# Optimization experiments

Hardware: AMD Instinct MI355X
Metric: run time of the kernel (lower is better)

## Reference

```python
import jax, jax.numpy as jnp
import numpy as np

BS = 2; D = 256; NH = 8; NL = 4; NP = 4; WS = 7; DFF = 1024
SHAPES = [(92, 92), (46, 46), (23, 23), (12, 12)]
LEN = sum(h * w for h, w in SHAPES)  # 11253
DH = D // NH


def _layer_norm(x, g, b):
    mu = jnp.mean(x, -1, keepdims=True)
    var = jnp.var(x, -1, keepdims=True)
    return (x - mu) * jax.lax.rsqrt(var + 1e-5) * g + b


def _bilinear(v_l, loc, H_, W_):
    # v_l: (N, nh, H_*W_, d); loc: (N, Lq, nh, P, 2) normalized in [0,1] (x, y)
    N, Lq, nh, P, _ = loc.shape
    x = loc[..., 0] * W_ - 0.5  # grid_sample align_corners=False convention
    y = loc[..., 1] * H_ - 0.5
    x0f = jnp.floor(x); y0f = jnp.floor(y)
    tx = (x - x0f).transpose(0, 2, 1, 3)  # (N, nh, Lq, P)
    ty = (y - y0f).transpose(0, 2, 1, 3)
    x0 = x0f.astype(jnp.int32).transpose(0, 2, 1, 3)
    y0 = y0f.astype(jnp.int32).transpose(0, 2, 1, 3)

    def g(yi, xi):
        valid = ((xi >= 0) & (xi < W_) & (yi >= 0) & (yi < H_)).astype(v_l.dtype)
        idx = (jnp.clip(yi, 0, H_ - 1) * W_ + jnp.clip(xi, 0, W_ - 1)).reshape(N, nh, Lq * P)
        out = jnp.take_along_axis(v_l, idx[..., None], axis=2).reshape(N, nh, Lq, P, -1)
        return out * valid[..., None]

    return (g(y0, x0) * ((1 - tx) * (1 - ty))[..., None]
            + g(y0, x0 + 1) * (tx * (1 - ty))[..., None]
            + g(y0 + 1, x0) * ((1 - tx) * ty)[..., None]
            + g(y0 + 1, x0 + 1) * (tx * ty)[..., None])


def setup_inputs() -> dict:
    key = jax.random.key(0)
    ks = jax.random.split(key, 20)
    s = 0.02
    inp = {}
    inp['src'] = jax.random.normal(ks[0], (BS, LEN, D), jnp.float32)
    inp['pos'] = jax.random.normal(ks[1], (BS, LEN, D), jnp.float32)
    inp['reference_points'] = jax.random.uniform(ks[2], (BS, LEN, NL, 2), jnp.float32)
    c = WS // 2
    ys, xs = jnp.meshgrid(jnp.arange(WS) - c, jnp.arange(WS) - c, indexing='ij')
    inp['window_grid'] = jnp.stack([xs, ys], -1).reshape(WS * WS, 2).astype(jnp.float32)
    for l, (h, w) in enumerate(SHAPES):
        inp[f'mask{l}'] = jax.random.normal(ks[3 + l], (BS, 1, h, w), jnp.float32)
    inp['spatial_shapes'] = jnp.array(SHAPES, jnp.int32)
    starts = np.cumsum([0] + [h * w for h, w in SHAPES])[:NL]
    inp['level_start_index'] = jnp.array(starts, jnp.int32)
    # parse_mask: Conv2d(1, n_heads, 1) per level -> per-head scale + bias
    inp['pm_w'] = jax.random.normal(ks[7], (NL, NH), jnp.float32) * s
    inp['pm_b'] = jax.random.normal(ks[8], (NL, NH), jnp.float32) * s
    inp['Wv'] = jax.random.normal(ks[9], (D, D), jnp.float32) * s
    inp['bv'] = jnp.zeros((D,), jnp.float32)
    inp['Wo'] = jax.random.normal(ks[10], (D, D), jnp.float32) * s
    inp['bo'] = jnp.zeros((D,), jnp.float32)
    inp['ln1_g'] = jnp.ones((D,), jnp.float32)
    inp['ln1_b'] = jnp.zeros((D,), jnp.float32)
    inp['W1'] = jax.random.normal(ks[11], (D, DFF), jnp.float32) * s
    inp['b1'] = jnp.zeros((DFF,), jnp.float32)
    inp['W2'] = jax.random.normal(ks[12], (DFF, D), jnp.float32) * s
    inp['b2'] = jnp.zeros((D,), jnp.float32)
    inp['ln2_g'] = jnp.ones((D,), jnp.float32)
    inp['ln2_b'] = jnp.zeros((D,), jnp.float32)
    return inp


def reference(src, pos, reference_points, window_grid, mask0, mask1, mask2, mask3,
              spatial_shapes, level_start_index, pm_w, pm_b, Wv, bv, Wo, bo,
              ln1_g, ln1_b, W1, b1, W2, b2, ln2_g, ln2_b):
    masks = [mask0, mask1, mask2, mask3]
    p = WS // 2
    offs, samp = [], []
    for l, (H_, W_) in enumerate(SHAPES):
        # 1x1 conv from 1 -> NH channels
        m = masks[l] * pm_w[l][None, :, None, None] + pm_b[l][None, :, None, None]  # (BS,NH,H,W)
        mp = jnp.pad(m, ((0, 0), (0, 0), (p, p), (p, p)))
        # unfold: (BS, NH, WS*WS, H*W), kernel positions row-major
        patches = jnp.stack([mp[:, :, i:i + H_, j:j + W_] for i in range(WS) for j in range(WS)], axis=2)
        patches = patches.reshape(BS, NH, WS * WS, H_ * W_).transpose(0, 1, 3, 2)  # (BS,NH,HW,WS^2)
        vals, idx = jax.lax.top_k(patches, NP)  # (BS,NH,HW,NP)
        off = window_grid[idx]  # (BS,NH,HW,NP,2)
        offs.append(off.transpose(0, 2, 1, 3, 4))   # (BS,HW,NH,NP,2)
        samp.append(vals.transpose(0, 2, 1, 3))     # (BS,HW,NH,NP)
    offsets = jnp.concatenate(offs, axis=1)       # (BS,LEN,NH,NP,2)
    pred_sampled = jnp.concatenate(samp, axis=1)  # (BS,LEN,NH,NP)

    # MSDeformAttn (encoder mode: external offsets + mask-derived attention logits)
    value = (src @ Wv + bv).reshape(BS, LEN, NH, DH)
    attn = jax.nn.softmax(
        jnp.broadcast_to(pred_sampled[:, :, :, None, :], (BS, LEN, NH, NL, NP)).reshape(BS, LEN, NH, NL * NP),
        axis=-1).reshape(BS, LEN, NH, NL, NP)
    norm = jnp.array([[w, h] for h, w in SHAPES], jnp.float32)  # (NL, 2) as (W, H)
    loc = reference_points[:, :, None, :, None, :] + offsets[:, :, :, None, :, :] / norm[None, None, None, :, None, :]

    out = jnp.zeros((BS, LEN, NH, DH), src.dtype)
    s0 = 0
    for l, (H_, W_) in enumerate(SHAPES):
        v_l = value[:, s0:s0 + H_ * W_].transpose(0, 2, 1, 3)  # (BS,NH,HW,DH)
        sampled = _bilinear(v_l, loc[:, :, :, l], H_, W_)       # (BS,NH,LEN,NP,DH)
        out = out + jnp.einsum('nhqpd,nqhp->nqhd', sampled, attn[:, :, :, l])
        s0 += H_ * W_
    attn_out = out.reshape(BS, LEN, D) @ Wo + bo

    x = _layer_norm(src + attn_out, ln1_g, ln1_b)
    x2 = jax.nn.relu(x @ W1 + b1) @ W2 + b2
    return _layer_norm(x + x2, ln2_g, ln2_b)
```

## Files before the change

kernel.cpp:

```cpp
#include <hip/hip_runtime.h>
#include <cstddef>
#include <cstdint>

#define LEN_T 11253
#define TOK   22506
#define NHEADS 8
#define DMODEL 256

typedef __attribute__((ext_vector_type(8))) short short8;
typedef __attribute__((ext_vector_type(4))) float f32x4;

__device__ __forceinline__ unsigned short f2bf(float f) {
  union { float f; unsigned u; } v; v.f = f;
  unsigned r = v.u + 0x7fffu + ((v.u >> 16) & 1u);
  return (unsigned short)(r >> 16);
}
__device__ __forceinline__ float bfhi2f(unsigned u) {
  union { unsigned u; float f; } v; v.u = u & 0xffff0000u; return v.f;
}
__device__ __forceinline__ float bflo2f(unsigned u) {
  union { unsigned u; float f; } v; v.u = u << 16; return v.f;
}

__device__ __forceinline__ void gld_lds16(const void* g, void* l) {
  __builtin_amdgcn_global_load_lds(
      (const __attribute__((address_space(1))) void*)g,
      (__attribute__((address_space(3))) void*)l, 16, 0, 0);
}

__global__ __launch_bounds__(256) void pre_kernel(
    const float* __restrict__ m0, const float* __restrict__ m1,
    const float* __restrict__ m2, const float* __restrict__ m3,
    const float* __restrict__ pm_w, const float* __restrict__ pm_b,
    const float* __restrict__ Wv, const float* __restrict__ Wo,
    const float* __restrict__ W1, const float* __restrict__ W2,
    unsigned short* __restrict__ Wv_t, unsigned short* __restrict__ Wo_t,
    unsigned short* __restrict__ W1_t, unsigned short* __restrict__ W2_t,
    unsigned* __restrict__ offp, float* __restrict__ attw)
{
  int blk = blockIdx.x;
  if (blk >= 704) {
    int cb = blk - 704;
    const float* W; unsigned short* Bt; int lk, ln, i;
    if (cb < 256)       { W = Wv; Bt = Wv_t; lk = 8;  ln = 8;  i = cb * 256 + threadIdx.x; }
    else if (cb < 512)  { W = Wo; Bt = Wo_t; lk = 8;  ln = 8;  i = (cb - 256) * 256 + threadIdx.x; }
    else if (cb < 1536) { W = W1; Bt = W1_t; lk = 8;  ln = 10; i = (cb - 512) * 256 + threadIdx.x; }
    else                { W = W2; Bt = W2_t; lk = 10; ln = 8;  i = (cb - 1536) * 256 + threadIdx.x; }
    int n = i >> lk;
    int k = i & ((1 << lk) - 1);
    Bt[i] = f2bf(W[((size_t)k << ln) + n]);
    return;
  }
  int t = blk * 256 + threadIdx.x;
  if (t >= TOK * NHEADS) return;
  int h  = t & 7;
  int bq = t >> 3;
  int b  = bq / LEN_T;
  int q  = bq - b * LEN_T;
  int l, H_, W_;
  const float* mk;
  if (q < 8464)       { l = 0; H_ = 92; W_ = 92; mk = m0; }
  else if (q < 10580) { l = 1; H_ = 46; W_ = 46; mk = m1; }
  else if (q < 11109) { l = 2; H_ = 23; W_ = 23; mk = m2; }
  else                { l = 3; H_ = 12; W_ = 12; mk = m3; }
  int st = (l == 0) ? 0 : (l == 1) ? 8464 : (l == 2) ? 10580 : 11109;
  int pos = q - st;
  int rr = pos / W_;
  int cc = pos - rr * W_;
  float w  = pm_w[l * NHEADS + h];
  float bb = pm_b[l * NHEADS + h];
  const float* mp = mk + (size_t)b * H_ * W_;

  float bestv[4] = {-1e30f, -1e30f, -1e30f, -1e30f};
  int   bestk[4] = {0, 0, 0, 0};
  for (int k = 0; k < 49; ++k) {
    int i = k / 7, j = k - (k / 7) * 7;
    int yy = rr + i - 3, xx = cc + j - 3;
    float v = 0.f;
    if (yy >= 0 && yy < H_ && xx >= 0 && xx < W_) v = mp[yy * W_ + xx] * w + bb;
    if (v > bestv[3]) {
      int p4 = 3;
      while (p4 > 0 && v > bestv[p4 - 1]) {
        bestv[p4] = bestv[p4 - 1]; bestk[p4] = bestk[p4 - 1]; --p4;
      }
      bestv[p4] = v; bestk[p4] = k;
    }
  }
  float mx = bestv[0];
  float ee[4];
  float s = 0.f;
  #pragma unroll
  for (int p = 0; p < 4; ++p) { ee[p] = __expf(bestv[p] - mx); s += ee[p]; }
  float inv = 1.f / (4.f * s);
  unsigned pk = 0;
  float* wp = attw + (size_t)t * 4;
  #pragma unroll
  for (int p = 0; p < 4; ++p) {
    int k = bestk[p];
    int i = k / 7, j = k - i * 7;
    pk |= (unsigned)(j | (i << 4)) << (8 * p);
    wp[p] = ee[p] * inv;
  }
  offp[t] = pk;
}

__global__ __launch_bounds__(256) void sample_kernel(
    const unsigned short* __restrict__ Vb, const float* __restrict__ refpts,
    const unsigned* __restrict__ offp, const float* __restrict__ attw,
    unsigned short* __restrict__ outp)
{
  __shared__ int4  sidx[4][128];
  __shared__ float4 swgt[4][128];
  const int wv   = threadIdx.x >> 6;
  const int lane = threadIdx.x & 63;
  const int bx = blockIdx.x & 7, by = blockIdx.x >> 3;
  const int nb = bx * 703 + min(bx, 3) + by;
  const int blk = nb * 4 + wv;
  const bool ok = blk < TOK;

  if (ok) {
    const int b = (blk >= LEN_T) ? 1 : 0;
    const float* rp = refpts + (size_t)blk * 8;
    #pragma unroll
    for (int e = 0; e < 2; ++e) {
      int t = lane * 2 + e;
      int h = t & 7, lp = t >> 3;
      int l = lp >> 2, p = lp & 3;
      unsigned pb = (offp[(size_t)blk * 8 + h] >> (8 * p)) & 0xffu;
      float ox = (float)(int)(pb & 15u) - 3.f;
      float oy = (float)(int)(pb >> 4)  - 3.f;
      float aw = attw[((size_t)blk * 8 + h) * 4 + p];
      int H_ = (l == 0) ? 92 : (l == 1) ? 46 : (l == 2) ? 23 : 12;
      int st = (l == 0) ? 0  : (l == 1) ? 8464 : (l == 2) ? 10580 : 11109;
      float xx = rp[2 * l]     * (float)H_ - 0.5f + ox;
      float yy = rp[2 * l + 1] * (float)H_ - 0.5f + oy;
      float x0f = floorf(xx), y0f = floorf(yy);
      float tx = xx - x0f, ty = yy - y0f;
      int x0 = (int)x0f, y0 = (int)y0f;
      int base = b * LEN_T + st;
      float wc[4] = {(1.f - tx) * (1.f - ty), tx * (1.f - ty),
                     (1.f - tx) * ty,         tx * ty};
      int4 idx; float4 wg;
      int xs[4] = {x0, x0 + 1, x0, x0 + 1};
      int ys[4] = {y0, y0, y0 + 1, y0 + 1};
      int   id[4]; float wgt[4];
      #pragma unroll
      for (int c = 0; c < 4; ++c) {
        int xi = xs[c], yi = ys[c];
        bool v_ = (xi >= 0) & (xi < H_) & (yi >= 0) & (yi < H_);
        id[c]  = base + min(max(yi, 0), H_ - 1) * H_ + min(max(xi, 0), H_ - 1);
        wgt[c] = v_ ? aw * wc[c] : 0.f;
      }
      idx.x = id[0]; idx.y = id[1]; idx.z = id[2]; idx.w = id[3];
      wg.x = wgt[0]; wg.y = wgt[1]; wg.z = wgt[2]; wg.w = wgt[3];
      sidx[wv][t] = idx;
      swgt[wv][t] = wg;
    }
  }
  __syncthreads();

  if (ok) {
    const int h = lane >> 3, dg = lane & 7;
    const unsigned short* vb = Vb + h * 32 + dg * 4;
    f32x4 acc = {0.f, 0.f, 0.f, 0.f};
    #pragma unroll 4
    for (int lp = 0; lp < 16; ++lp) {
      int4  idx = sidx[wv][lp * 8 + h];
      float4 wg = swgt[wv][lp * 8 + h];
      uint2 u0 = *(const uint2*)(vb + (size_t)idx.x * DMODEL);
      uint2 u1 = *(const uint2*)(vb + (size_t)idx.y * DMODEL);
      uint2 u2 = *(const uint2*)(vb + (size_t)idx.z * DMODEL);
      uint2 u3 = *(const uint2*)(vb + (size_t)idx.w * DMODEL);
      acc.x += wg.x * bflo2f(u0.x) + wg.y * bflo2f(u1.x) + wg.z * bflo2f(u2.x) + wg.w * bflo2f(u3.x);
      acc.y += wg.x * bfhi2f(u0.x) + wg.y * bfhi2f(u1.x) + wg.z * bfhi2f(u2.x) + wg.w * bfhi2f(u3.x);
      acc.z += wg.x * bflo2f(u0.y) + wg.y * bflo2f(u1.y) + wg.z * bflo2f(u2.y) + wg.w * bflo2f(u3.y);
      acc.w += wg.x * bfhi2f(u0.y) + wg.y * bfhi2f(u1.y) + wg.z * bfhi2f(u2.y) + wg.w * bfhi2f(u3.y);
    }
    uint2 o;
    o.x = (unsigned)f2bf(acc.x) | ((unsigned)f2bf(acc.y) << 16);
    o.y = (unsigned)f2bf(acc.z) | ((unsigned)f2bf(acc.w) << 16);
    *(uint2*)(outp + (size_t)blk * DMODEL + h * 32 + dg * 4) = o;
  }
}

template<int EPI, bool AF32>
__global__ __launch_bounds__(256, 2) void gemm_k256(
    const void* __restrict__ Aptr, const short* __restrict__ Bt,
    const float* __restrict__ bias, const float* __restrict__ res,
    const float* __restrict__ lng, const float* __restrict__ lnb,
    float* __restrict__ C, unsigned short* __restrict__ Cb,
    int M, int N)
{
  __shared__ short As[2][64 * 32] __attribute__((aligned(16)));
  __shared__ float2 lnred[64][4];
  const int tid  = threadIdx.x;
  const int w    = tid >> 6;
  const int lane = tid & 63;
  const int row0 = blockIdx.x * 64;
  const int wn   = blockIdx.y * 256 + w * 64;
  const int colq = lane & 15, quad = lane >> 4;
  const int kq8  = quad * 8;

  short8 bq[8][4];
  #pragma unroll
  for (int kc = 0; kc < 8; ++kc)
    #pragma unroll
    for (int nt = 0; nt < 4; ++nt)
      bq[kc][nt] = *(const short8*)(Bt + (size_t)(wn + nt * 16 + colq) * 256
                                       + kc * 32 + kq8);

  f32x4 acc[4][4];
  #pragma unroll
  for (int i = 0; i < 4; ++i)
    #pragma unroll
    for (int j = 0; j < 4; ++j) acc[i][j] = (f32x4){0.f, 0.f, 0.f, 0.f};

  const int rA  = min(row0 + (tid >> 2), M - 1);
  const int kq4 = (tid & 3) * 8;
  const float* Af = (const float*)Aptr;
  const short* Ab = (const short*)Aptr;

  auto stageA = [&](int kb, int nbuf) {
    if constexpr (AF32) {
      const float* ap = Af + (size_t)rA * 256 + kb * 32 + kq4;
      float4 f0 = *(const float4*)ap;
      float4 f1 = *(const float4*)(ap + 4);
      uint4 u;
      u.x = (unsigned)f2bf(f0.x) | ((unsigned)f2bf(f0.y) << 16);
      u.y = (unsigned)f2bf(f0.z) | ((unsigned)f2bf(f0.w) << 16);
      u.z = (unsigned)f2bf(f1.x) | ((unsigned)f2bf(f1.y) << 16);
      u.w = (unsigned)f2bf(f1.z) | ((unsigned)f2bf(f1.w) << 16);
      *(uint4*)(As[nbuf] + (size_t)tid * 8) = u;
    } else {
      gld_lds16(Ab + (size_t)rA * 256 + kb * 32 + kq4, As[nbuf] + (size_t)tid * 8);
    }
  };

  stageA(0, 0);
  __syncthreads();
  int buf = 0;
  #pragma unroll
  for (int kb = 0; kb < 8; ++kb) {
    if (kb < 7) stageA(kb + 1, buf ^ 1);
    short8 af[4];
    #pragma unroll
    for (int mt = 0; mt < 4; ++mt)
      af[mt] = *(const short8*)(As[buf] + (size_t)(mt * 16 + colq) * 32 + kq8);
    #pragma unroll
    for (int mt = 0; mt < 4; ++mt)
      #pragma unroll
      for (int nt = 0; nt < 4; ++nt)
        acc[mt][nt] = __builtin_amdgcn_mfma_f32_16x16x32_bf16(
            af[mt], bq[kb][nt], acc[mt][nt], 0, 0, 0);
    __syncthreads();
    buf ^= 1;
  }

  float bia[4];
  #pragma unroll
  for (int nt = 0; nt < 4; ++nt) bia[nt] = bias[wn + nt * 16 + colq];

  if constexpr (EPI == 1) {
    #pragma unroll
    for (int mt = 0; mt < 4; ++mt) {
      #pragma unroll
      for (int r = 0; r < 4; ++r) {
        int lrow = mt * 16 + quad * 4 + r;
        int rowc = min(row0 + lrow, M - 1);
        float s = 0.f, sq = 0.f;
        #pragma unroll
        for (int nt = 0; nt < 4; ++nt) {
          float f = acc[mt][nt][r] + bia[nt]
                  + res[(size_t)rowc * 256 + wn + nt * 16 + colq];
          acc[mt][nt][r] = f;
          s += f; sq += f * f;
        }
        #pragma unroll
        for (int off = 1; off < 16; off <<= 1) {
          s  += __shfl_xor(s,  off, 64);
          sq += __shfl_xor(sq, off, 64);
        }
        if (colq == 0) lnred[lrow][w] = (float2){s, sq};
      }
    }
    __syncthreads();
    #pragma unroll
    for (int mt = 0; mt < 4; ++mt) {
      #pragma unroll
      for (int r = 0; r < 4; ++r) {
        int lrow = mt * 16 + quad * 4 + r;
        int row  = row0 + lrow;
        if (row >= M) continue;
        float2 p0 = lnred[lrow][0], p1 = lnred[lrow][1];
        float2 p2 = lnred[lrow][2], p3 = lnred[lrow][3];
        float mu  = (p0.x + p1.x + p2.x + p3.x) * (1.f / 256.f);
        float var = (p0.y + p1.y + p2.y + p3.y) * (1.f / 256.f) - mu * mu;
        float rs  = rsqrtf(var + 1e-5f);
        #pragma unroll
        for (int nt = 0; nt < 4; ++nt) {
          int col = wn + nt * 16 + colq;
          float o = (acc[mt][nt][r] - mu) * rs * lng[col] + lnb[col];
          C[(size_t)row * 256 + col]  = o;
          Cb[(size_t)row * 256 + col] = f2bf(o);
        }
      }
    }
  } else {
    #pragma unroll
    for (int mt = 0; mt < 4; ++mt) {
      #pragma unroll
      for (int r = 0; r < 4; ++r) {
        int row = row0 + mt * 16 + quad * 4 + r;
        if (row < M) {
          #pragma unroll
          for (int nt = 0; nt < 4; ++nt) {
            float f = acc[mt][nt][r] + bia[nt];
            if constexpr (EPI == 2) f = fmaxf(f, 0.f);
            Cb[(size_t)row * N + wn + nt * 16 + colq] = f2bf(f);
          }
        }
      }
    }
  }
}

__global__ __launch_bounds__(256) void gemm_n256_ln(
    const short* __restrict__ A, const short* __restrict__ Bt,
    const float* __restrict__ bias, const float* __restrict__ res,
    const float* __restrict__ lng, const float* __restrict__ lnb,
    float* __restrict__ C, int M, int K)
{
  __shared__ short As[64 * 32]  __attribute__((aligned(16)));
  __shared__ short Bs[256 * 32] __attribute__((aligned(16)));
  __shared__ float2 lnred[64][2];
  const int tid  = threadIdx.x;
  const int w    = tid >> 6;
  const int lane = tid & 63;
  const int row0 = blockIdx.x * 64;

  f32x4 acc[2][8];
  #pragma unroll
  for (int i = 0; i < 2; ++i)
    #pragma unroll
    for (int j = 0; j < 8; ++j) acc[i][j] = (f32x4){0.f, 0.f, 0.f, 0.f};

  const int rA = min(row0 + (tid >> 2), M - 1);
  const short* ap = A + (size_t)rA * K + (tid & 3) * 8;
  short* lA = As + tid * 8;
  const short* bp[4]; short* lB[4];
  #pragma unroll
  for (int c = 0; c < 4; ++c) {
    int rB = c * 64 + (tid >> 2);
    bp[c] = Bt + (size_t)rB * K + (tid & 3) * 8;
    lB[c] = Bs + c * 2048 + tid * 8;
  }
  const int wm = (w & 1) * 32, wn = (w >> 1) * 128;
  const short* Abase = As + (size_t)(wm + (lane & 15)) * 32 + (lane >> 4) * 8;
  const short* Bbase = Bs + (size_t)(wn + (lane & 15)) * 32 + (lane >> 4) * 8;

  for (int kb = 0; kb < K; kb += 32) {
    gld_lds16(ap + kb, lA);
    #pragma unroll
    for (int c = 0; c < 4; ++c) gld_lds16(bp[c] + kb, lB[c]);
    __syncthreads();
    short8 af[2], bfr[8];
    #pragma unroll
    for (int mt = 0; mt < 2; ++mt) af[mt]  = *(const short8*)(Abase + mt * 16 * 32);
    #pragma unroll
    for (int nt = 0; nt < 8; ++nt) bfr[nt] = *(const short8*)(Bbase + nt * 16 * 32);
    #pragma unroll
    for (int mt = 0; mt < 2; ++mt)
      #pragma unroll
      for (int nt = 0; nt < 8; ++nt)
        acc[mt][nt] = __builtin_amdgcn_mfma_f32_16x16x32_bf16(
            af[mt], bfr[nt], acc[mt][nt], 0, 0, 0);
    __syncthreads();
  }

  const int colq = lane & 15, quad = lane >> 4;
  float bia[8];
  #pragma unroll
  for (int nt = 0; nt < 8; ++nt) bia[nt] = bias[wn + nt * 16 + colq];

  #pragma unroll
  for (int mt = 0; mt < 2; ++mt) {
    #pragma unroll
    for (int r = 0; r < 4; ++r) {
      int lrow = wm + mt * 16 + quad * 4 + r;
      int rowc = min(row0 + lrow, M - 1);
      float s = 0.f, sq = 0.f;
      #pragma unroll
      for (int nt = 0; nt < 8; ++nt) {
        float f = acc[mt][nt][r] + bia[nt]
                + res[(size_t)rowc * 256 + wn + nt * 16 + colq];
        acc[mt][nt][r] = f;
        s += f; sq += f * f;
      }
      #pragma unroll
      for (int off = 1; off < 16; off <<= 1) {
        s  += __shfl_xor(s,  off, 64);
        sq += __shfl_xor(sq, off, 64);
      }
      if (colq == 0) lnred[lrow][w >> 1] = (float2){s, sq};
    }
  }
  __syncthreads();
  #pragma unroll
  for (int mt = 0; mt < 2; ++mt) {
    #pragma unroll
    for (int r = 0; r < 4; ++r) {
      int lrow = wm + mt * 16 + quad * 4 + r;
      int row  = row0 + lrow;
      if (row >= M) continue;
      float2 p0 = lnred[lrow][0], p1 = lnred[lrow][1];
      float mu  = (p0.x + p1.x) * (1.f / 256.f);
      float var = (p0.y + p1.y) * (1.f / 256.f) - mu * mu;
      float rs  = rsqrtf(var + 1e-5f);
      #pragma unroll
      for (int nt = 0; nt < 8; ++nt) {
        int col = wn + nt * 16 + colq;
        C[(size_t)row * 256 + col] =
            (acc[mt][nt][r] - mu) * rs * lng[col] + lnb[col];
      }
    }
  }
}

extern "C" void kernel_launch(void* const* d_in, const int* in_sizes, int n_in,
                              void* d_out, int out_size, void* d_ws, size_t ws_size,
                              hipStream_t stream)
{
  const float* src    = (const float*)d_in[0];
  const float* refpts = (const float*)d_in[2];
  const float* m0   = (const float*)d_in[4];
  const float* m1   = (const float*)d_in[5];
  const float* m2   = (const float*)d_in[6];
  const float* m3   = (const float*)d_in[7];
  const float* pm_w = (const float*)d_in[10];
  const float* pm_b = (const float*)d_in[11];
  const float* Wv   = (const float*)d_in[12];
  const float* bv   = (const float*)d_in[13];
  const float* Wo   = (const float*)d_in[14];
  const float* bo   = (const float*)d_in[15];
  const float* W1   = (const float*)d_in[18];
  const float* b1   = (const float*)d_in[19];
  const float* W2   = (const float*)d_in[20];
  const float* b2   = (const float*)d_in[21];
  const float* ln1g = (const float*)d_in[16];
  const float* ln1b = (const float*)d_in[17];
  const float* ln2g = (const float*)d_in[22];
  const float* ln2b = (const float*)d_in[23];
  float* out = (float*)d_out;
  char*  w   = (char*)d_ws;

  const bool big = ws_size >= 97096256ull;
  const size_t H1SZ = big ? 46092288ull : 23046144ull;

  unsigned short* Vb      = (unsigned short*)(w);
  unsigned short* attnpre = (unsigned short*)(w + 11523072);
  float*          xf32    = (float*)(w + 23046144);
  unsigned short* h1      = (unsigned short*)(w + 46092288);
  char*           tail    = w + 46092288 + H1SZ;
  float*          attw    = (float*)(tail);
  unsigned*       offp    = (unsigned*)(tail + 2880768);
  unsigned short* Wv_t    = (unsigned short*)(tail + 3600960);
  unsigned short* Wo_t    = (unsigned short*)(tail + 3732032);
  unsigned short* W1_t    = (unsigned short*)(tail + 3863104);
  unsigned short* W2_t    = (unsigned short*)(tail + 4387392);
  unsigned short* x_bf    = attnpre;

  pre_kernel<<<dim3(3264), 256, 0, stream>>>(
      m0, m1, m2, m3, pm_w, pm_b, Wv, Wo, W1, W2,
      Wv_t, Wo_t, W1_t, W2_t, offp, attw);

  gemm_k256<0, true><<<dim3(352, 1), 256, 0, stream>>>(
      src, (const short*)Wv_t, bv, nullptr, nullptr, nullptr,
      nullptr, Vb, TOK, 256);

  sample_kernel<<<dim3(5627), 256, 0, stream>>>(
      Vb, refpts, offp, attw, attnpre);

  gemm_k256<1, false><<<dim3(352, 1), 256, 0, stream>>>(
      attnpre, (const short*)Wo_t, bo, src, ln1g, ln1b,
      xf32, x_bf, TOK, 256);

  if (big) {
    gemm_k256<2, false><<<dim3(352, 4), 256, 0, stream>>>(
        x_bf, (const short*)W1_t, b1, nullptr, nullptr, nullptr,
        nullptr, h1, TOK, 1024);
    gemm_n256_ln<<<dim3(352), 256, 0, stream>>>(
        (const short*)h1, (const short*)W2_t, b2, xf32, ln2g, ln2b,
        out, TOK, 1024);
  } else {
    for (int ch = 0; ch < 2; ++ch) {
      const unsigned short* xc = x_bf + (size_t)ch * LEN_T * 256;
      const float*          xr = xf32 + (size_t)ch * LEN_T * 256;
      float*                oc = out  + (size_t)ch * LEN_T * 256;
      gemm_k256<2, false><<<dim3(176, 4), 256, 0, stream>>>(
          xc, (const short*)W1_t, b1, nullptr, nullptr, nullptr,
          nullptr, h1, LEN_T, 1024);
      gemm_n256_ln<<<dim3(176), 256, 0, stream>>>(
          (const short*)h1, (const short*)W2_t, b2, xr, ln2g, ln2b,
          oc, LEN_T, 1024);
    }
  }
}
```

Baseline: 338.6 us.

## Restructure mask top-k, sampling, and FFN2 GEMM with register-resident B

The pre-kernel now handles one token per thread. For interior windows it computes the top-4 and bottom-4 of the 7x7 mask neighbourhood once and reuses them for all 8 heads, picking by the sign of the head weight (the bias cancels inside the softmax). Weight transposes write four elements per thread. The sampling kernel processes two tokens per wave with 16-byte value loads, 16-bit LDS indices, and occupancy hint 3. The separate FFN2 LDS-tiled GEMM is replaced by the register-resident-B GEMM generalised over K in chunks, which reloads B per 256-wide chunk. The trade-off is more register pressure and reloading B from global memory in FFN2.

```diff
diff --git a/kernel.cpp b/kernel.cpp
--- a/kernel.cpp
+++ b/kernel.cpp
@@ -21,11 +21,21 @@
 __device__ __forceinline__ float bflo2f(unsigned u) {
   union { unsigned u; float f; } v; v.u = u << 16; return v.f;
 }
-
 __device__ __forceinline__ void gld_lds16(const void* g, void* l) {
   __builtin_amdgcn_global_load_lds(
       (const __attribute__((address_space(1))) void*)g,
       (__attribute__((address_space(3))) void*)l, 16, 0, 0);
+}
+
+__device__ __forceinline__ void ins4(float v, int ji,
+    float& t0, float& t1, float& t2, float& t3,
+    int& i0, int& i1, int& i2, int& i3)
+{
+  bool a0 = v > t0, a1 = v > t1, a2 = v > t2, a3 = v > t3;
+  t3 = a3 ? (a2 ? t2 : v) : t3;  i3 = a3 ? (a2 ? i2 : ji) : i3;
+  t2 = a2 ? (a1 ? t1 : v) : t2;  i2 = a2 ? (a1 ? i1 : ji) : i2;
+  t1 = a1 ? (a0 ? t0 : v) : t1;  i1 = a1 ? (a0 ? i0 : ji) : i1;
+  t0 = a0 ? v : t0;              i0 = a0 ? ji : i0;
 }
 
 __global__ __launch_bounds__(256) void pre_kernel(
@@ -39,24 +49,28 @@
     unsigned* __restrict__ offp, float* __restrict__ attw)
 {
   int blk = blockIdx.x;
-  if (blk >= 704) {
-    int cb = blk - 704;
-    const float* W; unsigned short* Bt; int lk, ln, i;
-    if (cb < 256)       { W = Wv; Bt = Wv_t; lk = 8;  ln = 8;  i = cb * 256 + threadIdx.x; }
-    else if (cb < 512)  { W = Wo; Bt = Wo_t; lk = 8;  ln = 8;  i = (cb - 256) * 256 + threadIdx.x; }
-    else if (cb < 1536) { W = W1; Bt = W1_t; lk = 8;  ln = 10; i = (cb - 512) * 256 + threadIdx.x; }
-    else                { W = W2; Bt = W2_t; lk = 10; ln = 8;  i = (cb - 1536) * 256 + threadIdx.x; }
-    int n = i >> lk;
-    int k = i & ((1 << lk) - 1);
-    Bt[i] = f2bf(W[((size_t)k << ln) + n]);
+  if (blk >= 88) {
+    int cb = blk - 88;
+    const float* W; unsigned short* Bt; int lk, ln, base;
+    if (cb < 64)       { W = Wv; Bt = Wv_t; lk = 8;  ln = 8;  base = cb; }
+    else if (cb < 128) { W = Wo; Bt = Wo_t; lk = 8;  ln = 8;  base = cb - 64; }
+    else if (cb < 384) { W = W1; Bt = W1_t; lk = 8;  ln = 10; base = cb - 128; }
+    else               { W = W2; Bt = W2_t; lk = 10; ln = 8;  base = cb - 384; }
+    int i4 = (base * 256 + threadIdx.x) * 4;
+    int n  = i4 >> lk;
+    int k  = i4 & ((1 << lk) - 1);
+    ushort4 o;
+    o.x = f2bf(W[((size_t)(k + 0) << ln) + n]);
+    o.y = f2bf(W[((size_t)(k + 1) << ln) + n]);
+    o.z = f2bf(W[((size_t)(k + 2) << ln) + n]);
+    o.w = f2bf(W[((size_t)(k + 3) << ln) + n]);
+    *(ushort4*)(Bt + i4) = o;
     return;
   }
-  int t = blk * 256 + threadIdx.x;
-  if (t >= TOK * NHEADS) return;
-  int h  = t & 7;
-  int bq = t >> 3;
-  int b  = bq / LEN_T;
-  int q  = bq - b * LEN_T;
+  int tok = blk * 256 + threadIdx.x;
+  if (tok >= TOK) return;
+  int b = tok >= LEN_T;
+  int q = tok - b * LEN_T;
   int l, H_, W_;
   const float* mk;
   if (q < 8464)       { l = 0; H_ = 92; W_ = 92; mk = m0; }
@@ -67,130 +81,168 @@
   int pos = q - st;
   int rr = pos / W_;
   int cc = pos - rr * W_;
-  float w  = pm_w[l * NHEADS + h];
-  float bb = pm_b[l * NHEADS + h];
   const float* mp = mk + (size_t)b * H_ * W_;
-
-  float bestv[4] = {-1e30f, -1e30f, -1e30f, -1e30f};
-  int   bestk[4] = {0, 0, 0, 0};
-  for (int k = 0; k < 49; ++k) {
-    int i = k / 7, j = k - (k / 7) * 7;
-    int yy = rr + i - 3, xx = cc + j - 3;
-    float v = 0.f;
-    if (yy >= 0 && yy < H_ && xx >= 0 && xx < W_) v = mp[yy * W_ + xx] * w + bb;
-    if (v > bestv[3]) {
-      int p4 = 3;
-      while (p4 > 0 && v > bestv[p4 - 1]) {
-        bestv[p4] = bestv[p4 - 1]; bestk[p4] = bestk[p4 - 1]; --p4;
-      }
-      bestv[p4] = v; bestk[p4] = k;
-    }
-  }
-  float mx = bestv[0];
-  float ee[4];
-  float s = 0.f;
-  #pragma unroll
-  for (int p = 0; p < 4; ++p) { ee[p] = __expf(bestv[p] - mx); s += ee[p]; }
-  float inv = 1.f / (4.f * s);
-  unsigned pk = 0;
-  float* wp = attw + (size_t)t * 4;
-  #pragma unroll
-  for (int p = 0; p < 4; ++p) {
-    int k = bestk[p];
-    int i = k / 7, j = k - i * 7;
-    pk |= (unsigned)(j | (i << 4)) << (8 * p);
-    wp[p] = ee[p] * inv;
-  }
-  offp[t] = pk;
-}
-
-__global__ __launch_bounds__(256) void sample_kernel(
+  bool interior = (rr >= 3) && (rr + 3 < H_) && (cc >= 3) && (cc + 3 < W_);
+
+  if (interior) {
+    float t0=-1e30f,t1=-1e30f,t2=-1e30f,t3=-1e30f; int ti0=0,ti1=0,ti2=0,ti3=0;
+    float n0=-1e30f,n1=-1e30f,n2=-1e30f,n3=-1e30f; int bi0=0,bi1=0,bi2=0,bi3=0;
+    for (int i = 0; i < 7; ++i) {
+      const float* rowp = mp + (size_t)(rr + i - 3) * W_ + cc - 3;
+      #pragma unroll
+      for (int j = 0; j < 7; ++j) {
+        float v = rowp[j];
+        int ji = j | (i << 4);
+        ins4(v,  ji, t0, t1, t2, t3, ti0, ti1, ti2, ti3);
+        ins4(-v, ji, n0, n1, n2, n3, bi0, bi1, bi2, bi3);
+      }
+    }
+    unsigned pkt = (unsigned)ti0 | ((unsigned)ti1 << 8) | ((unsigned)ti2 << 16) | ((unsigned)ti3 << 24);
+    unsigned pkb = (unsigned)bi0 | ((unsigned)bi1 << 8) | ((unsigned)bi2 << 16) | ((unsigned)bi3 << 24);
+    #pragma unroll
+    for (int h = 0; h < 8; ++h) {
+      float w = pm_w[l * NHEADS + h];
+      bool neg = w < 0.f;
+      float v0 = neg ? -n0 : t0, v1 = neg ? -n1 : t1;
+      float v2 = neg ? -n2 : t2, v3 = neg ? -n3 : t3;
+      float e1 = __expf(w * (v1 - v0));
+      float e2 = __expf(w * (v2 - v0));
+      float e3 = __expf(w * (v3 - v0));
+      float inv = 1.f / (4.f * (1.f + e1 + e2 + e3));
+      float4 wout; wout.x = inv; wout.y = e1 * inv; wout.z = e2 * inv; wout.w = e3 * inv;
+      *(float4*)(attw + ((size_t)tok * 8 + h) * 4) = wout;
+      offp[(size_t)tok * 8 + h] = neg ? pkb : pkt;
+    }
+  } else {
+    #pragma unroll 1
+    for (int h = 0; h < 8; ++h) {
+      float w  = pm_w[l * NHEADS + h];
+      float bb = pm_b[l * NHEADS + h];
+      float t0=-1e30f,t1=-1e30f,t2=-1e30f,t3=-1e30f; int i0=0,i1=0,i2=0,i3=0;
+      for (int i = 0; i < 7; ++i) {
+        int yy = rr + i - 3;
+        #pragma unroll
+        for (int j = 0; j < 7; ++j) {
+          int xx = cc + j - 3;
+          float v = 0.f;
+          if (yy >= 0 && yy < H_ && xx >= 0 && xx < W_)
+            v = mp[(size_t)yy * W_ + xx] * w + bb;
+          ins4(v, j | (i << 4), t0, t1, t2, t3, i0, i1, i2, i3);
+        }
+      }
+      float e1 = __expf(t1 - t0);
+      float e2 = __expf(t2 - t0);
+      float e3 = __expf(t3 - t0);
+      float inv = 1.f / (4.f * (1.f + e1 + e2 + e3));
+      float4 wout; wout.x = inv; wout.y = e1 * inv; wout.z = e2 * inv; wout.w = e3 * inv;
+      *(float4*)(attw + ((size_t)tok * 8 + h) * 4) = wout;
+      offp[(size_t)tok * 8 + h] = (unsigned)i0 | ((unsigned)i1 << 8)
+                                | ((unsigned)i2 << 16) | ((unsigned)i3 << 24);
+    }
+  }
+}
+
+__global__ __launch_bounds__(256, 3) void sample_kernel(
     const unsigned short* __restrict__ Vb, const float* __restrict__ refpts,
     const unsigned* __restrict__ offp, const float* __restrict__ attw,
     unsigned short* __restrict__ outp)
 {
-  __shared__ int4  sidx[4][128];
-  __shared__ float4 swgt[4][128];
+  __shared__ ushort4 sidx[4][2][128];
+  __shared__ float4  swgt[4][2][128];
   const int wv   = threadIdx.x >> 6;
   const int lane = threadIdx.x & 63;
   const int bx = blockIdx.x & 7, by = blockIdx.x >> 3;
-  const int nb = bx * 703 + min(bx, 3) + by;
-  const int blk = nb * 4 + wv;
-  const bool ok = blk < TOK;
-
-  if (ok) {
-    const int b = (blk >= LEN_T) ? 1 : 0;
-    const float* rp = refpts + (size_t)blk * 8;
-    #pragma unroll
-    for (int e = 0; e < 2; ++e) {
-      int t = lane * 2 + e;
-      int h = t & 7, lp = t >> 3;
-      int l = lp >> 2, p = lp & 3;
-      unsigned pb = (offp[(size_t)blk * 8 + h] >> (8 * p)) & 0xffu;
+  const int nb = bx * 351 + min(bx, 6) + by;
+  const int base = nb * 8;
+
+  #pragma unroll
+  for (int e = 0; e < 4; ++e) {
+    int g  = lane * 4 + e;
+    int tk = g >> 7, t = g & 127;
+    int token = base + wv * 2 + tk;
+    ushort4 idx; idx.x = 0; idx.y = 0; idx.z = 0; idx.w = 0;
+    float4  wg;  wg.x = 0.f; wg.y = 0.f; wg.z = 0.f; wg.w = 0.f;
+    if (token < TOK) {
+      int h = t & 7, lp = t >> 3, lev = lp >> 2, p = lp & 3;
+      int b = token >= LEN_T;
+      unsigned pb = (offp[(size_t)token * 8 + h] >> (8 * p)) & 0xffu;
+      float aw = attw[((size_t)token * 8 + h) * 4 + p];
       float ox = (float)(int)(pb & 15u) - 3.f;
       float oy = (float)(int)(pb >> 4)  - 3.f;
-      float aw = attw[((size_t)blk * 8 + h) * 4 + p];
-      int H_ = (l == 0) ? 92 : (l == 1) ? 46 : (l == 2) ? 23 : 12;
-      int st = (l == 0) ? 0  : (l == 1) ? 8464 : (l == 2) ? 10580 : 11109;
-      float xx = rp[2 * l]     * (float)H_ - 0.5f + ox;
-      float yy = rp[2 * l + 1] * (float)H_ - 0.5f + oy;
+      int H_ = (lev == 0) ? 92 : (lev == 1) ? 46 : (lev == 2) ? 23 : 12;
+      int st = (lev == 0) ? 0  : (lev == 1) ? 8464 : (lev == 2) ? 10580 : 11109;
+      const float* rp = refpts + (size_t)token * 8;
+      float xx = rp[2 * lev]     * (float)H_ - 0.5f + ox;
+      float yy = rp[2 * lev + 1] * (float)H_ - 0.5f + oy;
       float x0f = floorf(xx), y0f = floorf(yy);
       float tx = xx - x0f, ty = yy - y0f;
       int x0 = (int)x0f, y0 = (int)y0f;
-      int base = b * LEN_T + st;
+      int vbase = b * LEN_T + st;
       float wc[4] = {(1.f - tx) * (1.f - ty), tx * (1.f - ty),
                      (1.f - tx) * ty,         tx * ty};
-      int4 idx; float4 wg;
       int xs[4] = {x0, x0 + 1, x0, x0 + 1};
       int ys[4] = {y0, y0, y0 + 1, y0 + 1};
-      int   id[4]; float wgt[4];
+      int id[4]; float wt[4];
       #pragma unroll
       for (int c = 0; c < 4; ++c) {
         int xi = xs[c], yi = ys[c];
         bool v_ = (xi >= 0) & (xi < H_) & (yi >= 0) & (yi < H_);
-        id[c]  = base + min(max(yi, 0), H_ - 1) * H_ + min(max(xi, 0), H_ - 1);
-        wgt[c] = v_ ? aw * wc[c] : 0.f;
-      }
-      idx.x = id[0]; idx.y = id[1]; idx.z = id[2]; idx.w = id[3];
-      wg.x = wgt[0]; wg.y = wgt[1]; wg.z = wgt[2]; wg.w = wgt[3];
-      sidx[wv][t] = idx;
-      swgt[wv][t] = wg;
-    }
+        id[c] = vbase + min(max(yi, 0), H_ - 1) * H_ + min(max(xi, 0), H_ - 1);
+        wt[c] = v_ ? aw * wc[c] : 0.f;
+      }
+      idx.x = (unsigned short)id[0]; idx.y = (unsigned short)id[1];
+      idx.z = (unsigned short)id[2]; idx.w = (unsigned short)id[3];
+      wg.x = wt[0]; wg.y = wt[1]; wg.z = wt[2]; wg.w = wt[3];
+    }
+    sidx[wv][tk][t] = idx;
+    swgt[wv][tk][t] = wg;
   }
   __syncthreads();
 
-  if (ok) {
-    const int h = lane >> 3, dg = lane & 7;
-    const unsigned short* vb = Vb + h * 32 + dg * 4;
-    f32x4 acc = {0.f, 0.f, 0.f, 0.f};
-    #pragma unroll 4
-    for (int lp = 0; lp < 16; ++lp) {
-      int4  idx = sidx[wv][lp * 8 + h];
-      float4 wg = swgt[wv][lp * 8 + h];
-      uint2 u0 = *(const uint2*)(vb + (size_t)idx.x * DMODEL);
-      uint2 u1 = *(const uint2*)(vb + (size_t)idx.y * DMODEL);
-      uint2 u2 = *(const uint2*)(vb + (size_t)idx.z * DMODEL);
-      uint2 u3 = *(const uint2*)(vb + (size_t)idx.w * DMODEL);
-      acc.x += wg.x * bflo2f(u0.x) + wg.y * bflo2f(u1.x) + wg.z * bflo2f(u2.x) + wg.w * bflo2f(u3.x);
-      acc.y += wg.x * bfhi2f(u0.x) + wg.y * bfhi2f(u1.x) + wg.z * bfhi2f(u2.x) + wg.w * bfhi2f(u3.x);
-      acc.z += wg.x * bflo2f(u0.y) + wg.y * bflo2f(u1.y) + wg.z * bflo2f(u2.y) + wg.w * bflo2f(u3.y);
-      acc.w += wg.x * bfhi2f(u0.y) + wg.y * bfhi2f(u1.y) + wg.z * bfhi2f(u2.y) + wg.w * bfhi2f(u3.y);
-    }
-    uint2 o;
-    o.x = (unsigned)f2bf(acc.x) | ((unsigned)f2bf(acc.y) << 16);
-    o.y = (unsigned)f2bf(acc.z) | ((unsigned)f2bf(acc.w) << 16);
-    *(uint2*)(outp + (size_t)blk * DMODEL + h * 32 + dg * 4) = o;
-  }
-}
-
-template<int EPI, bool AF32>
-__global__ __launch_bounds__(256, 2) void gemm_k256(
+  const int tk2 = lane >> 5;
+  const int h2  = (lane >> 2) & 7;
+  const int dg  = lane & 3;
+  const int token = base + wv * 2 + tk2;
+  ushort4 si[16];
+  #pragma unroll
+  for (int lp = 0; lp < 16; ++lp) si[lp] = sidx[wv][tk2][lp * 8 + h2];
+  const unsigned short* vb = Vb + h2 * 32 + dg * 8;
+  f32x4 aA = {0.f, 0.f, 0.f, 0.f}, aB = {0.f, 0.f, 0.f, 0.f};
+  #pragma unroll
+  for (int lp = 0; lp < 16; ++lp) {
+    float4 wg = swgt[wv][tk2][lp * 8 + h2];
+    uint4 u0 = *(const uint4*)(vb + (size_t)si[lp].x * DMODEL);
+    uint4 u1 = *(const uint4*)(vb + (size_t)si[lp].y * DMODEL);
+    uint4 u2 = *(const uint4*)(vb + (size_t)si[lp].z * DMODEL);
+    uint4 u3 = *(const uint4*)(vb + (size_t)si[lp].w * DMODEL);
+    aA.x += wg.x*bflo2f(u0.x) + wg.y*bflo2f(u1.x) + wg.z*bflo2f(u2.x) + wg.w*bflo2f(u3.x);
+    aA.y += wg.x*bfhi2f(u0.x) + wg.y*bfhi2f(u1.x) + wg.z*bfhi2f(u2.x) + wg.w*bfhi2f(u3.x);
+    aA.z += wg.x*bflo2f(u0.y) + wg.y*bflo2f(u1.y) + wg.z*bflo2f(u2.y) + wg.w*bflo2f(u3.y);
+    aA.w += wg.x*bfhi2f(u0.y) + wg.y*bfhi2f(u1.y) + wg.z*bfhi2f(u2.y) + wg.w*bfhi2f(u3.y);
+    aB.x += wg.x*bflo2f(u0.z) + wg.y*bflo2f(u1.z) + wg.z*bflo2f(u2.z) + wg.w*bflo2f(u3.z);
+    aB.y += wg.x*bfhi2f(u0.z) + wg.y*bfhi2f(u1.z) + wg.z*bfhi2f(u2.z) + wg.w*bfhi2f(u3.z);
+    aB.z += wg.x*bflo2f(u0.w) + wg.y*bflo2f(u1.w) + wg.z*bflo2f(u2.w) + wg.w*bflo2f(u3.w);
+    aB.w += wg.x*bfhi2f(u0.w) + wg.y*bfhi2f(u1.w) + wg.z*bfhi2f(u2.w) + wg.w*bfhi2f(u3.w);
+  }
+  if (token < TOK) {
+    uint4 o;
+    o.x = (unsigned)f2bf(aA.x) | ((unsigned)f2bf(aA.y) << 16);
+    o.y = (unsigned)f2bf(aA.z) | ((unsigned)f2bf(aA.w) << 16);
+    o.z = (unsigned)f2bf(aB.x) | ((unsigned)f2bf(aB.y) << 16);
+    o.w = (unsigned)f2bf(aB.z) | ((unsigned)f2bf(aB.w) << 16);
+    *(uint4*)(outp + (size_t)token * DMODEL + h2 * 32 + dg * 8) = o;
+  }
+}
+
+template<int EPI, bool AF32, int KC>
+__global__ __launch_bounds__(256, 2) void gemm_bres(
     const void* __restrict__ Aptr, const short* __restrict__ Bt,
     const float* __restrict__ bias, const float* __restrict__ res,
     const float* __restrict__ lng, const float* __restrict__ lnb,
     float* __restrict__ C, unsigned short* __restrict__ Cb,
     int M, int N)
 {
+  constexpr int K = KC * 256;
   __shared__ short As[2][64 * 32] __attribute__((aligned(16)));
   __shared__ float2 lnred[64][4];
   const int tid  = threadIdx.x;
@@ -202,12 +254,14 @@
   const int kq8  = quad * 8;
 
   short8 bq[8][4];
-  #pragma unroll
-  for (int kc = 0; kc < 8; ++kc)
-    #pragma unroll
-    for (int nt = 0; nt < 4; ++nt)
-      bq[kc][nt] = *(const short8*)(Bt + (size_t)(wn + nt * 16 + colq) * 256
-                                       + kc * 32 + kq8);
+  auto loadB = [&](int c) {
+    #pragma unroll
+    for (int kc = 0; kc < 8; ++kc)
+      #pragma unroll
+      for (int nt = 0; nt < 4; ++nt)
+        bq[kc][nt] = *(const short8*)(Bt + (size_t)(wn + nt * 16 + colq) * K
+                                         + c * 256 + kc * 32 + kq8);
+  };
 
   f32x4 acc[4][4];
   #pragma unroll
@@ -220,9 +274,9 @@
   const float* Af = (const float*)Aptr;
   const short* Ab = (const short*)Aptr;
 
-  auto stageA = [&](int kb, int nbuf) {
+  auto stageA = [&](int kbg, int nbuf) {
     if constexpr (AF32) {
-      const float* ap = Af + (size_t)rA * 256 + kb * 32 + kq4;
+      const float* ap = Af + (size_t)rA * K + kbg * 32 + kq4;
       float4 f0 = *(const float4*)ap;
       float4 f1 = *(const float4*)(ap + 4);
       uint4 u;
@@ -232,35 +286,41 @@
       u.w = (unsigned)f2bf(f1.z) | ((unsigned)f2bf(f1.w) << 16);
       *(uint4*)(As[nbuf] + (size_t)tid * 8) = u;
     } else {
-      gld_lds16(Ab + (size_t)rA * 256 + kb * 32 + kq4, As[nbuf] + (size_t)tid * 8);
+      gld_lds16(Ab + (size_t)rA * K + kbg * 32 + kq4, As[nbuf] + (size_t)tid * 8);
     }
   };
 
   stageA(0, 0);
+  loadB(0);
   __syncthreads();
   int buf = 0;
   #pragma unroll
-  for (int kb = 0; kb < 8; ++kb) {
-    if (kb < 7) stageA(kb + 1, buf ^ 1);
-    short8 af[4];
-    #pragma unroll
-    for (int mt = 0; mt < 4; ++mt)
-      af[mt] = *(const short8*)(As[buf] + (size_t)(mt * 16 + colq) * 32 + kq8);
-    #pragma unroll
-    for (int mt = 0; mt < 4; ++mt)
-      #pragma unroll
-      for (int nt = 0; nt < 4; ++nt)
-        acc[mt][nt] = __builtin_amdgcn_mfma_f32_16x16x32_bf16(
-            af[mt], bq[kb][nt], acc[mt][nt], 0, 0, 0);
-    __syncthreads();
-    buf ^= 1;
+  for (int c = 0; c < KC; ++c) {
+    if (c > 0) loadB(c);
+    #pragma unroll
+    for (int kb = 0; kb < 8; ++kb) {
+      const int kbg = c * 8 + kb;
+      if (kbg < KC * 8 - 1) stageA(kbg + 1, buf ^ 1);
+      short8 af[4];
+      #pragma unroll
+      for (int mt = 0; mt < 4; ++mt)
+        af[mt] = *(const short8*)(As[buf] + (size_t)(mt * 16 + colq) * 32 + kq8);
+      #pragma unroll
+      for (int mt = 0; mt < 4; ++mt)
+        #pragma unroll
+        for (int nt = 0; nt < 4; ++nt)
+          acc[mt][nt] = __builtin_amdgcn_mfma_f32_16x16x32_bf16(
+              af[mt], bq[kb][nt], acc[mt][nt], 0, 0, 0);
+      __syncthreads();
+      buf ^= 1;
+    }
   }
 
   float bia[4];
   #pragma unroll
   for (int nt = 0; nt < 4; ++nt) bia[nt] = bias[wn + nt * 16 + colq];
 
-  if constexpr (EPI == 1) {
+  if constexpr (EPI == 1 || EPI == 3) {
     #pragma unroll
     for (int mt = 0; mt < 4; ++mt) {
       #pragma unroll
@@ -300,8 +360,9 @@
         for (int nt = 0; nt < 4; ++nt) {
           int col = wn + nt * 16 + colq;
           float o = (acc[mt][nt][r] - mu) * rs * lng[col] + lnb[col];
-          C[(size_t)row * 256 + col]  = o;
-          Cb[(size_t)row * 256 + col] = f2bf(o);
+          C[(size_t)row * 256 + col] = o;
+          if constexpr (EPI == 1)
+            Cb[(size_t)row * 256 + col] = f2bf(o);
         }
       }
     }
@@ -319,108 +380,6 @@
             Cb[(size_t)row * N + wn + nt * 16 + colq] = f2bf(f);
           }
         }
-      }
-    }
-  }
-}
-
-__global__ __launch_bounds__(256) void gemm_n256_ln(
-    const short* __restrict__ A, const short* __restrict__ Bt,
-    const float* __restrict__ bias, const float* __restrict__ res,
-    const float* __restrict__ lng, const float* __restrict__ lnb,
-    float* __restrict__ C, int M, int K)
-{
-  __shared__ short As[64 * 32]  __attribute__((aligned(16)));
-  __shared__ short Bs[256 * 32] __attribute__((aligned(16)));
-  __shared__ float2 lnred[64][2];
-  const int tid  = threadIdx.x;
-  const int w    = tid >> 6;
-  const int lane = tid & 63;
-  const int row0 = blockIdx.x * 64;
-
-  f32x4 acc[2][8];
-  #pragma unroll
-  for (int i = 0; i < 2; ++i)
-    #pragma unroll
-    for (int j = 0; j < 8; ++j) acc[i][j] = (f32x4){0.f, 0.f, 0.f, 0.f};
-
-  const int rA = min(row0 + (tid >> 2), M - 1);
-  const short* ap = A + (size_t)rA * K + (tid & 3) * 8;
-  short* lA = As + tid * 8;
-  const short* bp[4]; short* lB[4];
-  #pragma unroll
-  for (int c = 0; c < 4; ++c) {
-    int rB = c * 64 + (tid >> 2);
-    bp[c] = Bt + (size_t)rB * K + (tid & 3) * 8;
-    lB[c] = Bs + c * 2048 + tid * 8;
-  }
-  const int wm = (w & 1) * 32, wn = (w >> 1) * 128;
-  const short* Abase = As + (size_t)(wm + (lane & 15)) * 32 + (lane >> 4) * 8;
-  const short* Bbase = Bs + (size_t)(wn + (lane & 15)) * 32 + (lane >> 4) * 8;
-
-  for (int kb = 0; kb < K; kb += 32) {
-    gld_lds16(ap + kb, lA);
-    #pragma unroll
-    for (int c = 0; c < 4; ++c) gld_lds16(bp[c] + kb, lB[c]);
-    __syncthreads();
-    short8 af[2], bfr[8];
-    #pragma unroll
-    for (int mt = 0; mt < 2; ++mt) af[mt]  = *(const short8*)(Abase + mt * 16 * 32);
-    #pragma unroll
-    for (int nt = 0; nt < 8; ++nt) bfr[nt] = *(const short8*)(Bbase + nt * 16 * 32);
-    #pragma unroll
-    for (int mt = 0; mt < 2; ++mt)
-      #pragma unroll
-      for (int nt = 0; nt < 8; ++nt)
-        acc[mt][nt] = __builtin_amdgcn_mfma_f32_16x16x32_bf16(
-            af[mt], bfr[nt], acc[mt][nt], 0, 0, 0);
-    __syncthreads();
-  }
-
-  const int colq = lane & 15, quad = lane >> 4;
-  float bia[8];
-  #pragma unroll
-  for (int nt = 0; nt < 8; ++nt) bia[nt] = bias[wn + nt * 16 + colq];
-
-  #pragma unroll
-  for (int mt = 0; mt < 2; ++mt) {
-    #pragma unroll
-    for (int r = 0; r < 4; ++r) {
-      int lrow = wm + mt * 16 + quad * 4 + r;
-      int rowc = min(row0 + lrow, M - 1);
-      float s = 0.f, sq = 0.f;
-      #pragma unroll
-      for (int nt = 0; nt < 8; ++nt) {
-        float f = acc[mt][nt][r] + bia[nt]
-                + res[(size_t)rowc * 256 + wn + nt * 16 + colq];
-        acc[mt][nt][r] = f;
-        s += f; sq += f * f;
-      }
-      #pragma unroll
-      for (int off = 1; off < 16; off <<= 1) {
-        s  += __shfl_xor(s,  off, 64);
-        sq += __shfl_xor(sq, off, 64);
-      }
-      if (colq == 0) lnred[lrow][w >> 1] = (float2){s, sq};
-    }
-  }
-  __syncthreads();
-  #pragma unroll
-  for (int mt = 0; mt < 2; ++mt) {
-    #pragma unroll
-    for (int r = 0; r < 4; ++r) {
-      int lrow = wm + mt * 16 + quad * 4 + r;
-      int row  = row0 + lrow;
-      if (row >= M) continue;
-      float2 p0 = lnred[lrow][0], p1 = lnred[lrow][1];
-      float mu  = (p0.x + p1.x) * (1.f / 256.f);
-      float var = (p0.y + p1.y) * (1.f / 256.f) - mu * mu;
-      float rs  = rsqrtf(var + 1e-5f);
-      #pragma unroll
-      for (int nt = 0; nt < 8; ++nt) {
-        int col = wn + nt * 16 + colq;
-        C[(size_t)row * 256 + col] =
-            (acc[mt][nt][r] - mu) * rs * lng[col] + lnb[col];
       }
     }
   }
@@ -442,12 +401,12 @@
   const float* bv   = (const float*)d_in[13];
   const float* Wo   = (const float*)d_in[14];
   const float* bo   = (const float*)d_in[15];
+  const float* ln1g = (const float*)d_in[16];
+  const float* ln1b = (const float*)d_in[17];
   const float* W1   = (const float*)d_in[18];
   const float* b1   = (const float*)d_in[19];
   const float* W2   = (const float*)d_in[20];
   const float* b2   = (const float*)d_in[21];
-  const float* ln1g = (const float*)d_in[16];
-  const float* ln1b = (const float*)d_in[17];
   const float* ln2g = (const float*)d_in[22];
   const float* ln2b = (const float*)d_in[23];
   float* out = (float*)d_out;
@@ -469,39 +428,39 @@
   unsigned short* W2_t    = (unsigned short*)(tail + 4387392);
   unsigned short* x_bf    = attnpre;
 
-  pre_kernel<<<dim3(3264), 256, 0, stream>>>(
+  pre_kernel<<<dim3(728), 256, 0, stream>>>(
       m0, m1, m2, m3, pm_w, pm_b, Wv, Wo, W1, W2,
       Wv_t, Wo_t, W1_t, W2_t, offp, attw);
 
-  gemm_k256<0, true><<<dim3(352, 1), 256, 0, stream>>>(
+  gemm_bres<0, true, 1><<<dim3(352, 1), 256, 0, stream>>>(
       src, (const short*)Wv_t, bv, nullptr, nullptr, nullptr,
       nullptr, Vb, TOK, 256);
 
-  sample_kernel<<<dim3(5627), 256, 0, stream>>>(
+  sample_kernel<<<dim3(2814), 256, 0, stream>>>(
       Vb, refpts, offp, attw, attnpre);
 
-  gemm_k256<1, false><<<dim3(352, 1), 256, 0, stream>>>(
+  gemm_bres<1, false, 1><<<dim3(352, 1), 256, 0, stream>>>(
       attnpre, (const short*)Wo_t, bo, src, ln1g, ln1b,
       xf32, x_bf, TOK, 256);
 
   if (big) {
-    gemm_k256<2, false><<<dim3(352, 4), 256, 0, stream>>>(
+    gemm_bres<2, false, 1><<<dim3(352, 4), 256, 0, stream>>>(
         x_bf, (const short*)W1_t, b1, nullptr, nullptr, nullptr,
         nullptr, h1, TOK, 1024);
-    gemm_n256_ln<<<dim3(352), 256, 0, stream>>>(
-        (const short*)h1, (const short*)W2_t, b2, xf32, ln2g, ln2b,
-        out, TOK, 1024);
+    gemm_bres<3, false, 4><<<dim3(352, 1), 256, 0, stream>>>(
+        h1, (const short*)W2_t, b2, xf32, ln2g, ln2b,
+        out, nullptr, TOK, 256);
   } else {
     for (int ch = 0; ch < 2; ++ch) {
       const unsigned short* xc = x_bf + (size_t)ch * LEN_T * 256;
       const float*          xr = xf32 + (size_t)ch * LEN_T * 256;
       float*                oc = out  + (size_t)ch * LEN_T * 256;
-      gemm_k256<2, false><<<dim3(176, 4), 256, 0, stream>>>(
+      gemm_bres<2, false, 1><<<dim3(176, 4), 256, 0, stream>>>(
           xc, (const short*)W1_t, b1, nullptr, nullptr, nullptr,
           nullptr, h1, LEN_T, 1024);
-      gemm_n256_ln<<<dim3(176), 256, 0, stream>>>(
-          (const short*)h1, (const short*)W2_t, b2, xr, ln2g, ln2b,
-          oc, LEN_T, 1024);
-    }
-  }
-}
+      gemm_bres<3, false, 4><<<dim3(176, 1), 256, 0, stream>>>(
+          h1, (const short*)W2_t, b2, xr, ln2g, ln2b,
+          oc, nullptr, LEN_T, 256);
+    }
+  }
+}
```

New measurement: 418.1 us. 1.23x slower.
